# Optimization experiments

Measured on AMD Instinct MI355X. Metric: run time of the kernel, lower is better.

## Reference

```python
import jax, jax.numpy as jnp
import numpy as np

NUM_USERS, NUM_ITEMS, D = 100000, 200000, 128
B, LLEN, SLEN = 4096, 200, 50
NEG = -1e9


def setup_inputs() -> dict:
    key = jax.random.key(0)
    ks = jax.random.split(key, 10)
    w_range = float(np.sqrt(3.0 / D))
    return {
        "user_table": 0.01 * jax.random.normal(ks[0], (NUM_USERS, D), dtype=jnp.float32),
        "item_table": 0.01 * jax.random.normal(ks[1], (NUM_ITEMS, D), dtype=jnp.float32),
        "W1": jax.random.uniform(ks[2], (2 * D, 16), minval=-w_range, maxval=w_range, dtype=jnp.float32),
        "b1": jnp.zeros((16,), dtype=jnp.float32),
        "W2": jax.random.uniform(ks[3], (16, 1), minval=-w_range, maxval=w_range, dtype=jnp.float32),
        "b2": jnp.zeros((1,), dtype=jnp.float32),
        "user_inputs": jax.random.randint(ks[4], (B,), 0, NUM_USERS, dtype=jnp.int64) if jax.config.jax_enable_x64 else jax.random.randint(ks[4], (B,), 0, NUM_USERS, dtype=jnp.int32),
        "L_inputs": jax.random.randint(ks[5], (B, LLEN), 0, NUM_ITEMS, dtype=jnp.int32),
        "S_inputs": jax.random.randint(ks[6], (B, SLEN), 0, NUM_ITEMS, dtype=jnp.int32),
        "item_inputs": jax.random.randint(ks[7], (B,), 0, NUM_ITEMS, dtype=jnp.int32),
    }


def reference(user_table, item_table, W1, b1, W2, b2,
              user_inputs, L_inputs, S_inputs, item_inputs):
    def att_logits(x):  # x: [..., 2D] -> [...]
        h = jax.nn.relu(x @ W1 + b1)
        return (h @ W2 + b2)[..., 0]

    def masked_softmax(logits, mask):  # softmax over last axis restricted to mask
        logits = jnp.where(mask, logits, NEG)
        return jax.nn.softmax(logits, axis=-1)

    u_emb = user_table[user_inputs]                      # [B, D]

    # ---- long-term attention over L history ----
    L_mask = L_inputs >= 0                               # [B, L]
    L_idx = jnp.where(L_mask, L_inputs, 0)
    L_emb = item_table[L_idx]                            # [B, L, D]
    uL = jnp.concatenate([jnp.broadcast_to(u_emb[:, None, :], L_emb.shape), L_emb], axis=-1)  # [B, L, 2D]
    w1 = masked_softmax(att_logits(uL), L_mask)          # [B, L]
    u_long = jnp.einsum('bl,bld->bd', w1, L_emb)         # [B, D]

    # ---- short-term attention over [u_long] + S (L assumed nonempty) ----
    S_mask = S_inputs >= 0                               # [B, S]
    S_idx = jnp.where(S_mask, S_inputs, 0)
    S_emb = item_table[S_idx]                            # [B, S, D]
    seq = jnp.concatenate([u_long[:, None, :], S_emb], axis=1)   # [B, 1+S, D]
    seq_mask = jnp.concatenate([jnp.ones((seq.shape[0], 1), dtype=bool), S_mask], axis=1)
    uSeq = jnp.concatenate([jnp.broadcast_to(u_emb[:, None, :], seq.shape), seq], axis=-1)  # [B, 1+S, 2D]
    w2 = masked_softmax(att_logits(uSeq), seq_mask)      # [B, 1+S]
    user_hybrid = jnp.einsum('bs,bsd->bd', w2, seq)      # [B, D]

    # ---- score: bmm([B,1,D], [B,D,1]) -> [B,1,1] ----
    item_emb = item_table[item_inputs]                   # [B, D]
    score = jnp.sum(user_hybrid * item_emb, axis=-1)[:, None, None]
    return score
```

## Files before the change

### kernel.cpp

```cpp
#include <hip/hip_runtime.h>
#include <math.h>

#define D 128
#define LLEN 200
#define SLEN 50
#define TSTR 136

typedef __attribute__((ext_vector_type(8))) short short8;
typedef __attribute__((ext_vector_type(4))) float f32x4;

__device__ __forceinline__ unsigned short f2bf(float f) {
  unsigned int u = __float_as_uint(f);
  return (unsigned short)((u + 0x7FFFu + ((u >> 16) & 1u)) >> 16);
}

__device__ __forceinline__ float wave_red_sum(float v) {
#pragma unroll
  for (int m = 32; m >= 1; m >>= 1) v += __shfl_xor(v, m, 64);
  return v;
}
__device__ __forceinline__ float block_sum(float v, float* red) {
  v = wave_red_sum(v);
  if ((threadIdx.x & 63) == 0) red[threadIdx.x >> 6] = v;
  __syncthreads();
  v = red[0] + red[1] + red[2] + red[3];
  __syncthreads();
  return v;
}

#define GATHER_L(dst, IT, BASE)                        \
  do {                                                 \
    int s_ = tid + (IT);                               \
    int gid_ = rows1[(BASE) + (s_ >> 5)];              \
    if (gid_ < 0) gid_ = 0;                            \
    dst = it4[(size_t)gid_ * 32 + (s_ & 31)];          \
  } while (0)

#define GATHER_S(dst, IT)                              \
  do {                                                 \
    int s_ = tid + (IT);                               \
    int gid_ = rowsS[s_ >> 5];                         \
    if (gid_ < 0) gid_ = 0;                            \
    dst = it4[(size_t)gid_ * 32 + (s_ & 31)];          \
  } while (0)

#define STOREB(src, IT, RO)                                                   \
  do {                                                                        \
    int s_ = tid + (IT);                                                      \
    ushort4 q_;                                                               \
    q_.x = f2bf(src.x); q_.y = f2bf(src.y);                                   \
    q_.z = f2bf(src.z); q_.w = f2bf(src.w);                                   \
    *reinterpret_cast<ushort4*>(&tb[((s_ >> 5) + (RO)) * TSTR +               \
                                    4 * (s_ & 31)]) = q_;                     \
  } while (0)

#define FMA4(WL, P, ACC)                \
  do {                                  \
    ACC.x = fmaf((WL), P.x, ACC.x);     \
    ACC.y = fmaf((WL), P.y, ACC.y);     \
    ACC.z = fmaf((WL), P.z, ACC.z);     \
  } while (0);                          \
  ACC.w = fmaf((WL), P.w, ACC.w)

template <int MODE>
__device__ __forceinline__ void mfma_logits(
    const unsigned short* tb, short8 Bf0, short8 Bf1, short8 Bf2, short8 Bf3,
    int w, int lane, float upart_j, float w2j, float b2v,
    const int* rowm, int nvalid, float* w_sh, float& pacc) {
  const int row = 16 * w + (lane & 15);
  const unsigned short* ap = &tb[row * TSTR + 8 * (lane >> 4)];
  short8 a0 = *reinterpret_cast<const short8*>(ap);
  short8 a1 = *reinterpret_cast<const short8*>(ap + 32);
  short8 a2 = *reinterpret_cast<const short8*>(ap + 64);
  short8 a3 = *reinterpret_cast<const short8*>(ap + 96);
  f32x4 acc = {0.f, 0.f, 0.f, 0.f};
  acc = __builtin_amdgcn_mfma_f32_16x16x32_bf16(a0, Bf0, acc, 0, 0, 0);
  acc = __builtin_amdgcn_mfma_f32_16x16x32_bf16(a1, Bf1, acc, 0, 0, 0);
  acc = __builtin_amdgcn_mfma_f32_16x16x32_bf16(a2, Bf2, acc, 0, 0, 0);
  acc = __builtin_amdgcn_mfma_f32_16x16x32_bf16(a3, Bf3, acc, 0, 0, 0);
  float v0 = fmaxf(upart_j + acc[0], 0.f) * w2j;
  float v1 = fmaxf(upart_j + acc[1], 0.f) * w2j;
  float v2 = fmaxf(upart_j + acc[2], 0.f) * w2j;
  float v3 = fmaxf(upart_j + acc[3], 0.f) * w2j;
#pragma unroll
  for (int m = 1; m <= 8; m <<= 1) {
    v0 += __shfl_xor(v0, m, 64);
    v1 += __shfl_xor(v1, m, 64);
    v2 += __shfl_xor(v2, m, 64);
    v3 += __shfl_xor(v3, m, 64);
  }
  if ((lane & 15) == 0) {
    const int it0 = 16 * w + 4 * (lane >> 4);
    float p0, p1, p2, p3;
    if (MODE == 0) {
      p0 = (it0 + 0 < nvalid && rowm[it0 + 0] >= 0) ? expf(v0 + b2v) : 0.f;
      p1 = (it0 + 1 < nvalid && rowm[it0 + 1] >= 0) ? expf(v1 + b2v) : 0.f;
      p2 = (it0 + 2 < nvalid && rowm[it0 + 2] >= 0) ? expf(v2 + b2v) : 0.f;
      p3 = (it0 + 3 < nvalid && rowm[it0 + 3] >= 0) ? expf(v3 + b2v) : 0.f;
    } else {
      p0 = (it0 == 0) ? expf(v0 + b2v)
                      : ((it0 < nvalid && rowm[it0 - 1] >= 0) ? expf(v0 + b2v) : 0.f);
      p1 = (it0 + 1 < nvalid && rowm[it0 + 0] >= 0) ? expf(v1 + b2v) : 0.f;
      p2 = (it0 + 2 < nvalid && rowm[it0 + 1] >= 0) ? expf(v2 + b2v) : 0.f;
      p3 = (it0 + 3 < nvalid && rowm[it0 + 2] >= 0) ? expf(v3 + b2v) : 0.f;
    }
    float4 pv;
    pv.x = p0; pv.y = p1; pv.z = p2; pv.w = p3;
    reinterpret_cast<float4*>(w_sh)[it0 >> 2] = pv;
    pacc += p0 + p1 + p2 + p3;
  }
}

__global__ void __launch_bounds__(256, 4) din_kernel(
    const float* __restrict__ user_table, const float* __restrict__ item_table,
    const float* __restrict__ W1, const float* __restrict__ b1,
    const float* __restrict__ W2, const float* __restrict__ b2,
    const int* __restrict__ user_inputs, const int* __restrict__ L_inputs,
    const int* __restrict__ S_inputs, const int* __restrict__ item_inputs,
    float* __restrict__ out) {
  __shared__ __align__(16) unsigned short tb[64 * TSTR];
  __shared__ __align__(16) float scratch[512];
  __shared__ __align__(16) float ul_sh[128];
  __shared__ __align__(16) float w_sh[64];
  __shared__ int rows1[LLEN];
  __shared__ int rowsS[SLEN];
  __shared__ float upart_sh[16];
  __shared__ float red_sh[4];

  const int b = blockIdx.x;
  const int tid = threadIdx.x;
  const int lane = tid & 63;
  const int w = __builtin_amdgcn_readfirstlane(tid >> 6);
  const int col4 = tid & 31;
  const int grp = tid >> 5;
  const float4* it4 = reinterpret_cast<const float4*>(item_table);

  float* u_sh = &scratch[0];
  float* part = &scratch[128];
  if (tid < D) u_sh[tid] = user_table[(size_t)user_inputs[b] * D + tid];
  const float item_f =
      (tid < D) ? item_table[(size_t)item_inputs[b] * D + tid] : 0.f;
  if (tid < LLEN) rows1[tid] = L_inputs[(size_t)b * LLEN + tid];
  if (tid < SLEN) rowsS[tid] = S_inputs[(size_t)b * SLEN + tid];
  __syncthreads();

  float4 A0, A1, A2, A3, A4, A5, A6, A7, B0, B1, B2, B3, B4, B5, B6, B7;
  GATHER_L(A0, 0, 0);    GATHER_L(A1, 256, 0);  GATHER_L(A2, 512, 0);
  GATHER_L(A3, 768, 0);  GATHER_L(A4, 1024, 0); GATHER_L(A5, 1280, 0);
  GATHER_L(A6, 1536, 0); GATHER_L(A7, 1792, 0);

  short8 Bf0, Bf1, Bf2, Bf3;
  {
    const int j = lane & 15, ko = lane >> 4;
    const float* wp = &W1[(size_t)(128 + 8 * ko) * 16 + j];
#pragma unroll
    for (int t = 0; t < 8; ++t) {
      Bf0[t] = (short)f2bf(wp[t * 16]);
      Bf1[t] = (short)f2bf(wp[(32 + t) * 16]);
      Bf2[t] = (short)f2bf(wp[(64 + t) * 16]);
      Bf3[t] = (short)f2bf(wp[(96 + t) * 16]);
    }
  }

  {
    int j = tid & 15, g = tid >> 4;
    float p = 0.f;
#pragma unroll
    for (int t = 0; t < 8; ++t) {
      int d = g * 8 + t;
      p = fmaf(u_sh[d], W1[d * 16 + j], p);
    }
    part[tid] = p;
  }
  __syncthreads();
  if (tid < 16) {
    float s = b1[tid];
#pragma unroll
    for (int g = 0; g < 16; ++g) s += part[g * 16 + tid];
    upart_sh[tid] = s;
  }
  __syncthreads();

  const float b2v = b2[0];
  const float upart_j = upart_sh[lane & 15];
  const float w2j = W2[lane & 15];

  float pacc = 0.f;
  float4 uacc = make_float4(0.f, 0.f, 0.f, 0.f);
  float wl;

  STOREB(A0, 0, 0);    STOREB(A1, 256, 0);  STOREB(A2, 512, 0);
  STOREB(A3, 768, 0);  STOREB(A4, 1024, 0); STOREB(A5, 1280, 0);
  STOREB(A6, 1536, 0); STOREB(A7, 1792, 0);
  GATHER_L(B0, 0, 64);    GATHER_L(B1, 256, 64);  GATHER_L(B2, 512, 64);
  GATHER_L(B3, 768, 64);  GATHER_L(B4, 1024, 64); GATHER_L(B5, 1280, 64);
  GATHER_L(B6, 1536, 64); GATHER_L(B7, 1792, 64);
  __syncthreads();
  mfma_logits<0>(tb, Bf0, Bf1, Bf2, Bf3, w, lane, upart_j, w2j, b2v,
                 rows1 + 0, 64, w_sh, pacc);
  __syncthreads();
  wl = w_sh[grp];      FMA4(wl, A0, uacc);
  wl = w_sh[grp + 8];  FMA4(wl, A1, uacc);
  wl = w_sh[grp + 16]; FMA4(wl, A2, uacc);
  wl = w_sh[grp + 24]; FMA4(wl, A3, uacc);
  wl = w_sh[grp + 32]; FMA4(wl, A4, uacc);
  wl = w_sh[grp + 40]; FMA4(wl, A5, uacc);
  wl = w_sh[grp + 48]; FMA4(wl, A6, uacc);
  wl = w_sh[grp + 56]; FMA4(wl, A7, uacc);

  STOREB(B0, 0, 0);    STOREB(B1, 256, 0);  STOREB(B2, 512, 0);
  STOREB(B3, 768, 0);  STOREB(B4, 1024, 0); STOREB(B5, 1280, 0);
  STOREB(B6, 1536, 0); STOREB(B7, 1792, 0);
  GATHER_L(A0, 0, 128);    GATHER_L(A1, 256, 128);  GATHER_L(A2, 512, 128);
  GATHER_L(A3, 768, 128);  GATHER_L(A4, 1024, 128); GATHER_L(A5, 1280, 128);
  GATHER_L(A6, 1536, 128); GATHER_L(A7, 1792, 128);
  __syncthreads();
  mfma_logits<0>(tb, Bf0, Bf1, Bf2, Bf3, w, lane, upart_j, w2j, b2v,
                 rows1 + 64, 64, w_sh, pacc);
  __syncthreads();
  wl = w_sh[grp];      FMA4(wl, B0, uacc);
  wl = w_sh[grp + 8];  FMA4(wl, B1, uacc);
  wl = w_sh[grp + 16]; FMA4(wl, B2, uacc);
  wl = w_sh[grp + 24]; FMA4(wl, B3, uacc);
  wl = w_sh[grp + 32]; FMA4(wl, B4, uacc);
  wl = w_sh[grp + 40]; FMA4(wl, B5, uacc);
  wl = w_sh[grp + 48]; FMA4(wl, B6, uacc);
  wl = w_sh[grp + 56]; FMA4(wl, B7, uacc);

  STOREB(A0, 0, 0);    STOREB(A1, 256, 0);  STOREB(A2, 512, 0);
  STOREB(A3, 768, 0);  STOREB(A4, 1024, 0); STOREB(A5, 1280, 0);
  STOREB(A6, 1536, 0); STOREB(A7, 1792, 0);
  GATHER_L(B0, 0, 192);
  GATHER_S(B1, 0);    GATHER_S(B2, 256);  GATHER_S(B3, 512);
  GATHER_S(B4, 768);  GATHER_S(B5, 1024); GATHER_S(B6, 1280);
  if (tid < 64) GATHER_S(B7, 1536);
  __syncthreads();
  mfma_logits<0>(tb, Bf0, Bf1, Bf2, Bf3, w, lane, upart_j, w2j, b2v,
                 rows1 + 128, 64, w_sh, pacc);
  __syncthreads();
  wl = w_sh[grp];      FMA4(wl, A0, uacc);
  wl = w_sh[grp + 8];  FMA4(wl, A1, uacc);
  wl = w_sh[grp + 16]; FMA4(wl, A2, uacc);
  wl = w_sh[grp + 24]; FMA4(wl, A3, uacc);
  wl = w_sh[grp + 32]; FMA4(wl, A4, uacc);
  wl = w_sh[grp + 40]; FMA4(wl, A5, uacc);
  wl = w_sh[grp + 48]; FMA4(wl, A6, uacc);
  wl = w_sh[grp + 56]; FMA4(wl, A7, uacc);

  STOREB(B0, 0, 0);
  __syncthreads();
  if (w == 0)
    mfma_logits<0>(tb, Bf0, Bf1, Bf2, Bf3, w, lane, upart_j, w2j, b2v,
                   rows1 + 192, 8, w_sh, pacc);
  __syncthreads();
  wl = w_sh[grp];
  FMA4(wl, B0, uacc);

  const float invS1 = 1.f / block_sum(pacc, red_sh);
  uacc.x += __shfl_xor(uacc.x, 32, 64);
  uacc.y += __shfl_xor(uacc.y, 32, 64);
  uacc.z += __shfl_xor(uacc.z, 32, 64);
  uacc.w += __shfl_xor(uacc.w, 32, 64);
  if (lane < 32) reinterpret_cast<float4*>(scratch)[(w << 5) + lane] = uacc;
  STOREB(B1, 0, 1);    STOREB(B2, 256, 1);  STOREB(B3, 512, 1);
  STOREB(B4, 768, 1);  STOREB(B5, 1024, 1); STOREB(B6, 1280, 1);
  if (tid < 64) STOREB(B7, 1536, 1);
  __syncthreads();
  if (tid < D) {
    float s = scratch[tid] + scratch[128 + tid] + scratch[256 + tid] +
              scratch[384 + tid];
    float ul = s * invS1;
    ul_sh[tid] = ul;
    tb[tid] = f2bf(ul);
  }
  __syncthreads();

  float pacc2 = 0.f;
  mfma_logits<1>(tb, Bf0, Bf1, Bf2, Bf3, w, lane, upart_j, w2j, b2v,
                 rowsS, 51, w_sh, pacc2);
  const float invS2 = 1.f / block_sum(pacc2, red_sh);

  float4 uacc2 = make_float4(0.f, 0.f, 0.f, 0.f);
  if (grp == 0) {
    float wl0 = w_sh[0];
    const float4 e = reinterpret_cast<const float4*>(ul_sh)[col4];
    FMA4(wl0, e, uacc2);
  }
  wl = w_sh[1 + grp];  FMA4(wl, B1, uacc2);
  wl = w_sh[9 + grp];  FMA4(wl, B2, uacc2);
  wl = w_sh[17 + grp]; FMA4(wl, B3, uacc2);
  wl = w_sh[25 + grp]; FMA4(wl, B4, uacc2);
  wl = w_sh[33 + grp]; FMA4(wl, B5, uacc2);
  wl = w_sh[41 + grp]; FMA4(wl, B6, uacc2);
  if (grp < 2) { wl = w_sh[49 + grp]; FMA4(wl, B7, uacc2); }

  uacc2.x += __shfl_xor(uacc2.x, 32, 64);
  uacc2.y += __shfl_xor(uacc2.y, 32, 64);
  uacc2.z += __shfl_xor(uacc2.z, 32, 64);
  uacc2.w += __shfl_xor(uacc2.w, 32, 64);
  if (lane < 32) reinterpret_cast<float4*>(scratch)[(w << 5) + lane] = uacc2;
  __syncthreads();

  float sv = 0.f;
  if (tid < D) {
    float s = scratch[tid] + scratch[128 + tid] + scratch[256 + tid] +
              scratch[384 + tid];
    sv = s * invS2 * item_f;
  }
  float tot = block_sum(sv, red_sh);
  if (tid == 0) out[b] = tot;
}

extern "C" void kernel_launch(void* const* d_in, const int* in_sizes, int n_in,
                              void* d_out, int out_size, void* d_ws, size_t ws_size,
                              hipStream_t stream) {
  const float* user_table = (const float*)d_in[0];
  const float* item_table = (const float*)d_in[1];
  const float* W1 = (const float*)d_in[2];
  const float* b1 = (const float*)d_in[3];
  const float* W2 = (const float*)d_in[4];
  const float* b2 = (const float*)d_in[5];
  const int* user_inputs = (const int*)d_in[6];
  const int* L_inputs = (const int*)d_in[7];
  const int* S_inputs = (const int*)d_in[8];
  const int* item_inputs = (const int*)d_in[9];
  float* out = (float*)d_out;

  const int B = in_sizes[6];
  din_kernel<<<B, 256, 0, stream>>>(user_table, item_table, W1, b1, W2, b2,
                                    user_inputs, L_inputs, S_inputs, item_inputs,
                                    out);
}
```

Baseline: 297.5 us.

## Stage gathered rows as fp32 in LDS and read them back for weighted sum

The LDS tile now stores gathered embeddings as fp32 (stride 132) instead of bf16. The MFMA path converts them to bf16 when it loads them, and the weighted-sum pass re-reads the rows from LDS. Before, the gathered float4s were held in registers across the double-buffer. This drops the second register bank (A/B to a single P set) and folds the three chunks into a rolled loop, aiming to cut VGPR pressure and code size. In exchange, LDS use roughly doubles, which may limit occupancy, and each chunk costs extra LDS reads and a barrier.

```diff
diff --git a/kernel.cpp b/kernel.cpp
--- a/kernel.cpp
+++ b/kernel.cpp
@@ -4,7 +4,7 @@
 #define D 128
 #define LLEN 200
 #define SLEN 50
-#define TSTR 136
+#define ESTR 132
 
 typedef __attribute__((ext_vector_type(8))) short short8;
 typedef __attribute__((ext_vector_type(4))) float f32x4;
@@ -44,14 +44,16 @@
     dst = it4[(size_t)gid_ * 32 + (s_ & 31)];          \
   } while (0)
 
-#define STOREB(src, IT, RO)                                                   \
-  do {                                                                        \
-    int s_ = tid + (IT);                                                      \
-    ushort4 q_;                                                               \
-    q_.x = f2bf(src.x); q_.y = f2bf(src.y);                                   \
-    q_.z = f2bf(src.z); q_.w = f2bf(src.w);                                   \
-    *reinterpret_cast<ushort4*>(&tb[((s_ >> 5) + (RO)) * TSTR +               \
-                                    4 * (s_ & 31)]) = q_;                     \
+#define STORE_L(src, IT)                                                     \
+  do {                                                                       \
+    int s_ = tid + (IT);                                                     \
+    reinterpret_cast<float4*>(&ebuf[(s_ >> 5) * ESTR])[s_ & 31] = src;       \
+  } while (0)
+
+#define STORE_S(src, IT)                                                     \
+  do {                                                                       \
+    int s_ = tid + (IT);                                                     \
+    reinterpret_cast<float4*>(&ebuf[((s_ >> 5) + 1) * ESTR])[s_ & 31] = src; \
   } while (0)
 
 #define FMA4(WL, P, ACC)                \
@@ -62,17 +64,28 @@
   } while (0);                          \
   ACC.w = fmaf((WL), P.w, ACC.w)
 
+#define PACK8(DST, FA, FB)                                 \
+  do {                                                     \
+    DST[0] = (short)f2bf(FA.x); DST[1] = (short)f2bf(FA.y);\
+    DST[2] = (short)f2bf(FA.z); DST[3] = (short)f2bf(FA.w);\
+    DST[4] = (short)f2bf(FB.x); DST[5] = (short)f2bf(FB.y);\
+    DST[6] = (short)f2bf(FB.z); DST[7] = (short)f2bf(FB.w);\
+  } while (0)
+
 template <int MODE>
 __device__ __forceinline__ void mfma_logits(
-    const unsigned short* tb, short8 Bf0, short8 Bf1, short8 Bf2, short8 Bf3,
+    const float* eb, short8 Bf0, short8 Bf1, short8 Bf2, short8 Bf3,
     int w, int lane, float upart_j, float w2j, float b2v,
     const int* rowm, int nvalid, float* w_sh, float& pacc) {
   const int row = 16 * w + (lane & 15);
-  const unsigned short* ap = &tb[row * TSTR + 8 * (lane >> 4)];
-  short8 a0 = *reinterpret_cast<const short8*>(ap);
-  short8 a1 = *reinterpret_cast<const short8*>(ap + 32);
-  short8 a2 = *reinterpret_cast<const short8*>(ap + 64);
-  short8 a3 = *reinterpret_cast<const short8*>(ap + 96);
+  const float4* ap4 =
+      reinterpret_cast<const float4*>(&eb[row * ESTR + 8 * (lane >> 4)]);
+  float4 f0 = ap4[0], f1 = ap4[1];
+  float4 f2 = ap4[8], f3 = ap4[9];
+  float4 f4 = ap4[16], f5 = ap4[17];
+  float4 f6 = ap4[24], f7 = ap4[25];
+  short8 a0, a1, a2, a3;
+  PACK8(a0, f0, f1); PACK8(a1, f2, f3); PACK8(a2, f4, f5); PACK8(a3, f6, f7);
   f32x4 acc = {0.f, 0.f, 0.f, 0.f};
   acc = __builtin_amdgcn_mfma_f32_16x16x32_bf16(a0, Bf0, acc, 0, 0, 0);
   acc = __builtin_amdgcn_mfma_f32_16x16x32_bf16(a1, Bf1, acc, 0, 0, 0);
@@ -118,9 +131,7 @@
     const int* __restrict__ user_inputs, const int* __restrict__ L_inputs,
     const int* __restrict__ S_inputs, const int* __restrict__ item_inputs,
     float* __restrict__ out) {
-  __shared__ __align__(16) unsigned short tb[64 * TSTR];
-  __shared__ __align__(16) float scratch[512];
-  __shared__ __align__(16) float ul_sh[128];
+  __shared__ __align__(16) float ebuf[64 * ESTR];
   __shared__ __align__(16) float w_sh[64];
   __shared__ int rows1[LLEN];
   __shared__ int rowsS[SLEN];
@@ -135,8 +146,8 @@
   const int grp = tid >> 5;
   const float4* it4 = reinterpret_cast<const float4*>(item_table);
 
-  float* u_sh = &scratch[0];
-  float* part = &scratch[128];
+  float* u_sh = &ebuf[0];
+  float* part = &ebuf[128];
   if (tid < D) u_sh[tid] = user_table[(size_t)user_inputs[b] * D + tid];
   const float item_f =
       (tid < D) ? item_table[(size_t)item_inputs[b] * D + tid] : 0.f;
@@ -144,10 +155,10 @@
   if (tid < SLEN) rowsS[tid] = S_inputs[(size_t)b * SLEN + tid];
   __syncthreads();
 
-  float4 A0, A1, A2, A3, A4, A5, A6, A7, B0, B1, B2, B3, B4, B5, B6, B7;
-  GATHER_L(A0, 0, 0);    GATHER_L(A1, 256, 0);  GATHER_L(A2, 512, 0);
-  GATHER_L(A3, 768, 0);  GATHER_L(A4, 1024, 0); GATHER_L(A5, 1280, 0);
-  GATHER_L(A6, 1536, 0); GATHER_L(A7, 1792, 0);
+  float4 P0, P1, P2, P3, P4, P5, P6, P7;
+  GATHER_L(P0, 0, 0);    GATHER_L(P1, 256, 0);  GATHER_L(P2, 512, 0);
+  GATHER_L(P3, 768, 0);  GATHER_L(P4, 1024, 0); GATHER_L(P5, 1280, 0);
+  GATHER_L(P6, 1536, 0); GATHER_L(P7, 1792, 0);
 
   short8 Bf0, Bf1, Bf2, Bf3;
   {
@@ -189,122 +200,95 @@
   float4 uacc = make_float4(0.f, 0.f, 0.f, 0.f);
   float wl;
 
-  STOREB(A0, 0, 0);    STOREB(A1, 256, 0);  STOREB(A2, 512, 0);
-  STOREB(A3, 768, 0);  STOREB(A4, 1024, 0); STOREB(A5, 1280, 0);
-  STOREB(A6, 1536, 0); STOREB(A7, 1792, 0);
-  GATHER_L(B0, 0, 64);    GATHER_L(B1, 256, 64);  GATHER_L(B2, 512, 64);
-  GATHER_L(B3, 768, 64);  GATHER_L(B4, 1024, 64); GATHER_L(B5, 1280, 64);
-  GATHER_L(B6, 1536, 64); GATHER_L(B7, 1792, 64);
-  __syncthreads();
-  mfma_logits<0>(tb, Bf0, Bf1, Bf2, Bf3, w, lane, upart_j, w2j, b2v,
-                 rows1 + 0, 64, w_sh, pacc);
-  __syncthreads();
-  wl = w_sh[grp];      FMA4(wl, A0, uacc);
-  wl = w_sh[grp + 8];  FMA4(wl, A1, uacc);
-  wl = w_sh[grp + 16]; FMA4(wl, A2, uacc);
-  wl = w_sh[grp + 24]; FMA4(wl, A3, uacc);
-  wl = w_sh[grp + 32]; FMA4(wl, A4, uacc);
-  wl = w_sh[grp + 40]; FMA4(wl, A5, uacc);
-  wl = w_sh[grp + 48]; FMA4(wl, A6, uacc);
-  wl = w_sh[grp + 56]; FMA4(wl, A7, uacc);
-
-  STOREB(B0, 0, 0);    STOREB(B1, 256, 0);  STOREB(B2, 512, 0);
-  STOREB(B3, 768, 0);  STOREB(B4, 1024, 0); STOREB(B5, 1280, 0);
-  STOREB(B6, 1536, 0); STOREB(B7, 1792, 0);
-  GATHER_L(A0, 0, 128);    GATHER_L(A1, 256, 128);  GATHER_L(A2, 512, 128);
-  GATHER_L(A3, 768, 128);  GATHER_L(A4, 1024, 128); GATHER_L(A5, 1280, 128);
-  GATHER_L(A6, 1536, 128); GATHER_L(A7, 1792, 128);
-  __syncthreads();
-  mfma_logits<0>(tb, Bf0, Bf1, Bf2, Bf3, w, lane, upart_j, w2j, b2v,
-                 rows1 + 64, 64, w_sh, pacc);
-  __syncthreads();
-  wl = w_sh[grp];      FMA4(wl, B0, uacc);
-  wl = w_sh[grp + 8];  FMA4(wl, B1, uacc);
-  wl = w_sh[grp + 16]; FMA4(wl, B2, uacc);
-  wl = w_sh[grp + 24]; FMA4(wl, B3, uacc);
-  wl = w_sh[grp + 32]; FMA4(wl, B4, uacc);
-  wl = w_sh[grp + 40]; FMA4(wl, B5, uacc);
-  wl = w_sh[grp + 48]; FMA4(wl, B6, uacc);
-  wl = w_sh[grp + 56]; FMA4(wl, B7, uacc);
-
-  STOREB(A0, 0, 0);    STOREB(A1, 256, 0);  STOREB(A2, 512, 0);
-  STOREB(A3, 768, 0);  STOREB(A4, 1024, 0); STOREB(A5, 1280, 0);
-  STOREB(A6, 1536, 0); STOREB(A7, 1792, 0);
-  GATHER_L(B0, 0, 192);
-  GATHER_S(B1, 0);    GATHER_S(B2, 256);  GATHER_S(B3, 512);
-  GATHER_S(B4, 768);  GATHER_S(B5, 1024); GATHER_S(B6, 1280);
-  if (tid < 64) GATHER_S(B7, 1536);
-  __syncthreads();
-  mfma_logits<0>(tb, Bf0, Bf1, Bf2, Bf3, w, lane, upart_j, w2j, b2v,
-                 rows1 + 128, 64, w_sh, pacc);
-  __syncthreads();
-  wl = w_sh[grp];      FMA4(wl, A0, uacc);
-  wl = w_sh[grp + 8];  FMA4(wl, A1, uacc);
-  wl = w_sh[grp + 16]; FMA4(wl, A2, uacc);
-  wl = w_sh[grp + 24]; FMA4(wl, A3, uacc);
-  wl = w_sh[grp + 32]; FMA4(wl, A4, uacc);
-  wl = w_sh[grp + 40]; FMA4(wl, A5, uacc);
-  wl = w_sh[grp + 48]; FMA4(wl, A6, uacc);
-  wl = w_sh[grp + 56]; FMA4(wl, A7, uacc);
-
-  STOREB(B0, 0, 0);
+#pragma unroll 1
+  for (int c = 0; c < 3; ++c) {
+    const int base = c * 64;
+    STORE_L(P0, 0);    STORE_L(P1, 256);  STORE_L(P2, 512);  STORE_L(P3, 768);
+    STORE_L(P4, 1024); STORE_L(P5, 1280); STORE_L(P6, 1536); STORE_L(P7, 1792);
+    __syncthreads();
+    if (c < 2) {
+      GATHER_L(P0, 0, base + 64);    GATHER_L(P1, 256, base + 64);
+      GATHER_L(P2, 512, base + 64);  GATHER_L(P3, 768, base + 64);
+      GATHER_L(P4, 1024, base + 64); GATHER_L(P5, 1280, base + 64);
+      GATHER_L(P6, 1536, base + 64); GATHER_L(P7, 1792, base + 64);
+    } else {
+      GATHER_L(P0, 0, 192);
+      GATHER_S(P1, 0);    GATHER_S(P2, 256);  GATHER_S(P3, 512);
+      GATHER_S(P4, 768);  GATHER_S(P5, 1024); GATHER_S(P6, 1280);
+      if (tid < 64) GATHER_S(P7, 1536);
+    }
+    mfma_logits<0>(ebuf, Bf0, Bf1, Bf2, Bf3, w, lane, upart_j, w2j, b2v,
+                   rows1 + base, 64, w_sh, pacc);
+    __syncthreads();
+#pragma unroll
+    for (int i = 0; i < 8; ++i) {
+      int l = grp + 8 * i;
+      wl = w_sh[l];
+      const float4 e = reinterpret_cast<const float4*>(&ebuf[l * ESTR])[col4];
+      FMA4(wl, e, uacc);
+    }
+    __syncthreads();
+  }
+
+  STORE_L(P0, 0);
   __syncthreads();
   if (w == 0)
-    mfma_logits<0>(tb, Bf0, Bf1, Bf2, Bf3, w, lane, upart_j, w2j, b2v,
+    mfma_logits<0>(ebuf, Bf0, Bf1, Bf2, Bf3, w, lane, upart_j, w2j, b2v,
                    rows1 + 192, 8, w_sh, pacc);
   __syncthreads();
   wl = w_sh[grp];
-  FMA4(wl, B0, uacc);
+  {
+    const float4 e = reinterpret_cast<const float4*>(&ebuf[grp * ESTR])[col4];
+    FMA4(wl, e, uacc);
+  }
 
   const float invS1 = 1.f / block_sum(pacc, red_sh);
   uacc.x += __shfl_xor(uacc.x, 32, 64);
   uacc.y += __shfl_xor(uacc.y, 32, 64);
   uacc.z += __shfl_xor(uacc.z, 32, 64);
   uacc.w += __shfl_xor(uacc.w, 32, 64);
-  if (lane < 32) reinterpret_cast<float4*>(scratch)[(w << 5) + lane] = uacc;
-  STOREB(B1, 0, 1);    STOREB(B2, 256, 1);  STOREB(B3, 512, 1);
-  STOREB(B4, 768, 1);  STOREB(B5, 1024, 1); STOREB(B6, 1280, 1);
-  if (tid < 64) STOREB(B7, 1536, 1);
+  float* scr = &ebuf[52 * ESTR];
+  if (lane < 32) reinterpret_cast<float4*>(scr)[(w << 5) + lane] = uacc;
+  STORE_S(P1, 0);    STORE_S(P2, 256);  STORE_S(P3, 512);
+  STORE_S(P4, 768);  STORE_S(P5, 1024); STORE_S(P6, 1280);
+  if (tid < 64) STORE_S(P7, 1536);
   __syncthreads();
   if (tid < D) {
-    float s = scratch[tid] + scratch[128 + tid] + scratch[256 + tid] +
-              scratch[384 + tid];
-    float ul = s * invS1;
-    ul_sh[tid] = ul;
-    tb[tid] = f2bf(ul);
+    float s = scr[tid] + scr[128 + tid] + scr[256 + tid] + scr[384 + tid];
+    ebuf[tid] = s * invS1;
   }
   __syncthreads();
 
   float pacc2 = 0.f;
-  mfma_logits<1>(tb, Bf0, Bf1, Bf2, Bf3, w, lane, upart_j, w2j, b2v,
+  mfma_logits<1>(ebuf, Bf0, Bf1, Bf2, Bf3, w, lane, upart_j, w2j, b2v,
                  rowsS, 51, w_sh, pacc2);
   const float invS2 = 1.f / block_sum(pacc2, red_sh);
 
   float4 uacc2 = make_float4(0.f, 0.f, 0.f, 0.f);
-  if (grp == 0) {
-    float wl0 = w_sh[0];
-    const float4 e = reinterpret_cast<const float4*>(ul_sh)[col4];
-    FMA4(wl0, e, uacc2);
-  }
-  wl = w_sh[1 + grp];  FMA4(wl, B1, uacc2);
-  wl = w_sh[9 + grp];  FMA4(wl, B2, uacc2);
-  wl = w_sh[17 + grp]; FMA4(wl, B3, uacc2);
-  wl = w_sh[25 + grp]; FMA4(wl, B4, uacc2);
-  wl = w_sh[33 + grp]; FMA4(wl, B5, uacc2);
-  wl = w_sh[41 + grp]; FMA4(wl, B6, uacc2);
-  if (grp < 2) { wl = w_sh[49 + grp]; FMA4(wl, B7, uacc2); }
+#pragma unroll
+  for (int i = 0; i < 6; ++i) {
+    int l = grp + 8 * i;
+    wl = w_sh[l];
+    const float4 e = reinterpret_cast<const float4*>(&ebuf[l * ESTR])[col4];
+    FMA4(wl, e, uacc2);
+  }
+  if (grp < 3) {
+    int l = 48 + grp;
+    wl = w_sh[l];
+    const float4 e = reinterpret_cast<const float4*>(&ebuf[l * ESTR])[col4];
+    FMA4(wl, e, uacc2);
+  }
 
   uacc2.x += __shfl_xor(uacc2.x, 32, 64);
   uacc2.y += __shfl_xor(uacc2.y, 32, 64);
   uacc2.z += __shfl_xor(uacc2.z, 32, 64);
   uacc2.w += __shfl_xor(uacc2.w, 32, 64);
-  if (lane < 32) reinterpret_cast<float4*>(scratch)[(w << 5) + lane] = uacc2;
+  if (lane < 32) reinterpret_cast<float4*>(scr)[(w << 5) + lane] = uacc2;
   __syncthreads();
 
   float sv = 0.f;
   if (tid < D) {
-    float s = scratch[tid] + scratch[128 + tid] + scratch[256 + tid] +
-              scratch[384 + tid];
+    float s = scr[tid] + scr[128 + tid] + scr[256 + tid] + scr[384 + tid];
     sv = s * invS2 * item_f;
   }
   float tot = block_sum(sv, red_sh);
```

Result: faster. 268.7 us (-9.7%).
